# Kernel tuning notes

Hardware: AMD Instinct MI355X
Metric: run time of the kernel (lower is better)

## Reference

```python
import jax, jax.numpy as jnp
import numpy as np

STRIDE, PADDING, EPS = 2, 1, 1e-5


def setup_inputs() -> dict:
    key = jax.random.key(0)
    k1, k2, k3 = jax.random.split(key, 3)
    C_in, C_out, K = 64, 64, 4
    x = jax.random.normal(k1, (32, C_in, 64, 64), dtype=jnp.float32)
    weight = jax.random.normal(k2, (C_in, C_out, K, K), dtype=jnp.float32) * 0.05  # torch layout (in,out,kh,kw)
    conv_bias = jax.random.normal(k3, (C_out,), dtype=jnp.float32) * 0.02
    gamma = jnp.ones((C_out,), dtype=jnp.float32)
    beta = jnp.zeros((C_out,), dtype=jnp.float32)
    running_mean = jnp.zeros((C_out,), dtype=jnp.float32)
    running_var = jnp.ones((C_out,), dtype=jnp.float32)
    return {"x": x, "weight": weight, "conv_bias": conv_bias, "gamma": gamma,
            "beta": beta, "running_mean": running_mean, "running_var": running_var}


def _conv_transpose2d(x, weight, bias, stride, padding):
    # torch.nn.functional.conv_transpose2d equivalent:
    # conv with lhs_dilation=stride, spatially-flipped kernel, in/out axes swapped,
    # and padding k-1-p on each side.
    k = weight.shape[2]
    w_t = jnp.transpose(jnp.flip(weight, (2, 3)), (1, 0, 2, 3))  # (Cout, Cin, k, k)
    pad = k - 1 - padding
    y = jax.lax.conv_general_dilated(
        x, w_t,
        window_strides=(1, 1),
        padding=[(pad, pad), (pad, pad)],
        lhs_dilation=(stride, stride),
        dimension_numbers=("NCHW", "OIHW", "NCHW"),
    )
    return y + bias[None, :, None, None]


def reference(x, weight, conv_bias, gamma, beta, running_mean, running_var):
    # ConvTranspose2d
    y = _conv_transpose2d(x, weight, conv_bias, STRIDE, PADDING)  # [N,C,128,128]
    # BatchNorm2d (inference, running stats)
    scale = gamma * jax.lax.rsqrt(running_var + EPS)
    y = (y - running_mean[None, :, None, None]) * scale[None, :, None, None] + beta[None, :, None, None]
    # Softmax over channel dim
    y = jax.nn.softmax(y, axis=1)
    # MaxPool2d(k=2, s=2): H,W are even, so reshape-max is exact
    N, C, H, W = y.shape
    y = y.reshape(N, C, H // 2, 2, W // 2, 2).max(axis=(3, 5))  # [N,C,64,64]
    return y
```

## Files before the change

kernel.cpp:

```cpp
#include <hip/hip_runtime.h>
#include <hip/hip_bf16.h>
#include <math.h>


typedef __attribute__((ext_vector_type(8))) short short8;
typedef __attribute__((ext_vector_type(4))) float floatx4;
typedef __attribute__((ext_vector_type(2))) unsigned uint2v;

__device__ ushort g_wfrag[4 * 8 * 4 * 64 * 8];
__device__ float g_aff[64];

#define L2E 1.44269504088896340736f

__device__ __forceinline__ ushort f2bf(float f) {
  union { float f; unsigned u; } v; v.f = f;
  unsigned r = v.u + 0x7FFF + ((v.u >> 16) & 1);
  return (ushort)(r >> 16);
}

__global__ __launch_bounds__(256) void prep_kernel(
    const float* __restrict__ w, const float* __restrict__ bias,
    const float* __restrict__ gamma, const float* __restrict__ beta,
    const float* __restrict__ mean, const float* __restrict__ var) {
  int t = blockIdx.x * 256 + threadIdx.x;
  int cin0 = (t >> 6) * 2;
  int cout = t & 63;
  int nt = cout >> 4, b15 = cout & 15;
  int q = (cin0 & 31) >> 3;
  int j = cin0 & 7;
  int ksq = cin0 >> 5;
  float Aw = gamma[cout] * rsqrtf(var[cout] + 1e-5f) * L2E;

  const float4* p0 = (const float4*)&w[(cin0 * 64 + cout) * 16];
  const float4* p1 = (const float4*)&w[((cin0 + 1) * 64 + cout) * 16];
  float a[16], b[16];
  {
    float4 f0 = p0[0], f1 = p0[1], f2 = p0[2], f3 = p0[3];
    a[0]=f0.x; a[1]=f0.y; a[2]=f0.z; a[3]=f0.w; a[4]=f1.x; a[5]=f1.y; a[6]=f1.z; a[7]=f1.w;
    a[8]=f2.x; a[9]=f2.y; a[10]=f2.z; a[11]=f2.w; a[12]=f3.x; a[13]=f3.y; a[14]=f3.z; a[15]=f3.w;
    float4 g0 = p1[0], g1 = p1[1], g2 = p1[2], g3 = p1[3];
    b[0]=g0.x; b[1]=g0.y; b[2]=g0.z; b[3]=g0.w; b[4]=g1.x; b[5]=g1.y; b[6]=g1.z; b[7]=g1.w;
    b[8]=g2.x; b[9]=g2.y; b[10]=g2.z; b[11]=g2.w; b[12]=g3.x; b[13]=g3.y; b[14]=g3.z; b[15]=g3.w;
  }
#pragma unroll
  for (int kh = 0; kh < 4; ++kh)
#pragma unroll
    for (int kw = 0; kw < 4; ++kw) {
      int r = (kh & 1) ? 0 : 1;
      int pp = (kw & 1) ? 0 : 1;
      int c = r * 2 + pp;
      int tap = (kh >> 1) * 2 + (kw >> 1);
      int ks = tap * 2 + ksq;
      unsigned u = (unsigned)f2bf(a[kh * 4 + kw] * Aw) |
                   ((unsigned)f2bf(b[kh * 4 + kw] * Aw) << 16);
      *(unsigned*)&g_wfrag[(((c * 8 + ks) * 4 + nt) * 64 + q * 16 + b15) * 8 + j] = u;
    }

  if (t < 64) {
    float A0 = gamma[t] * rsqrtf(var[t] + 1e-5f);
    g_aff[t] = ((bias[t] - mean[t]) * A0 + beta[t]) * L2E;
  }
}

__device__ __forceinline__ unsigned cvtpk(float a, float b) {
  unsigned r;
  asm("v_cvt_pk_bf16_f32 %0, %1, %2" : "=v"(r) : "v"(a), "v"(b));
  return r;
}

template <int CTRL>
__device__ __forceinline__ float dpp_add(float v) {
  unsigned t = (unsigned)__builtin_amdgcn_update_dpp(
      0, (int)__float_as_uint(v), CTRL, 0xF, 0xF, true);
  return v + __uint_as_float(t);
}

__device__ __forceinline__ float sum16(float v) {
  v = dpp_add<0xB1>(v);
  v = dpp_add<0x4E>(v);
  v = dpp_add<0x141>(v);
  v = dpp_add<0x140>(v);
  return v;
}

__device__ __forceinline__ float fexp2(float x) {
#if __has_builtin(__builtin_amdgcn_exp2f)
  return __builtin_amdgcn_exp2f(x);
#else
  return exp2f(x);
#endif
}

__device__ __forceinline__ void gload_lds16(const void* g, void* l) {
  __builtin_amdgcn_global_load_lds(
      (const __attribute__((address_space(1))) void*)g,
      (__attribute__((address_space(3))) void*)l, 16, 0, 0);
}

#define COLS 66
#define ROWSTRIDE (COLS * 64)

__global__ __launch_bounds__(512, 4) void fused_kernel(const float* __restrict__ x,
                                                       float* __restrict__ out) {
  __shared__ __align__(16) ushort xs[4 * ROWSTRIDE];
  __shared__ __align__(16) float red[2 * 64 * 65 + 16];

  ushort* wbuf = (ushort*)red;

  const int tid  = threadIdx.x;
  const int swz  = ((blockIdx.x & 7) << 2) | (blockIdx.x >> 3);
  const int ph0  = swz * 2;
  const int n    = blockIdx.y;
  const int wave = tid >> 6;
  const int lane = tid & 63;
  const int b15  = lane & 15;
  const int q    = lane >> 4;
  const int wc   = wave & 1;
  const int c    = wave >> 1;
  const int r    = c >> 1, p = c & 1;

#define STAGE_W(ks_)                                                          \
  {                                                                           \
    _Pragma("unroll")                                                         \
    for (int nt_ = 0; nt_ < 4; ++nt_)                                         \
      gload_lds16(&g_wfrag[(((c * 8 + (ks_)) * 4 + nt_) * 64 + lane) * 8],    \
                  &wbuf[(wave * 4 + nt_) * 512]);                             \
  }
  STAGE_W(0);

  for (int e = tid; e < 1024; e += 512) {
    int iw4 = e & 15;
    int c4  = (e >> 4) & 15;
    int row = e >> 8;
    int ih  = ph0 - 1 + row;
    float4 v0 = {0.f, 0.f, 0.f, 0.f}, v1 = v0, v2 = v0, v3 = v0;
    if (ih >= 0 && ih < 64) {
      const float* xp = x + ((n * 64 + c4 * 4) * 64 + ih) * 64 + iw4 * 4;
      v0 = *(const float4*)xp;          v1 = *(const float4*)(xp + 4096);
      v2 = *(const float4*)(xp + 8192); v3 = *(const float4*)(xp + 12288);
    }
    int chunk = c4 >> 1, half4 = (c4 & 1) * 4;
    float cc[4][4] = {{v0.x, v1.x, v2.x, v3.x}, {v0.y, v1.y, v2.y, v3.y},
                      {v0.z, v1.z, v2.z, v3.z}, {v0.w, v1.w, v2.w, v3.w}};
#pragma unroll
    for (int ii = 0; ii < 4; ++ii) {
      int col = iw4 * 4 + ii + 1;
      uint2v pk = {cvtpk(cc[ii][0], cc[ii][1]), cvtpk(cc[ii][2], cc[ii][3])};
      *(uint2v*)&xs[(row * COLS + col) * 64 + ((chunk ^ (col & 7)) * 8) + half4] = pk;
    }
  }
  for (int e = tid; e < 128; e += 512) {
    int c4 = e & 15, side = (e >> 4) & 1, row = e >> 5;
    int col = side ? 65 : 0;
    int chunk = c4 >> 1, half4 = (c4 & 1) * 4;
    ushort4 z; z.x = z.y = z.z = z.w = 0;
    *(ushort4*)&xs[(row * COLS + col) * 64 + ((chunk ^ (col & 7)) * 8) + half4] = z;
  }

  float Dc[4];
#pragma unroll
  for (int nt = 0; nt < 4; ++nt) Dc[nt] = g_aff[nt * 16 + b15];

  int A2[2][2];
#pragma unroll
  for (int b = 0; b < 2; ++b) {
    int col = wc * 32 + b15 + (b ? p - 1 : p) + 1;
#pragma unroll
    for (int par = 0; par < 2; ++par)
      A2[b][par] = r * ROWSTRIDE + col * 64 + (((par * 4 + q) ^ (col & 7)) * 8);
  }

  __syncthreads();

  floatx4 acc[16];
#pragma unroll
  for (int i = 0; i < 16; ++i) {
    float d = Dc[i & 3];
    acc[i] = (floatx4){d, d, d, d};
  }

#pragma unroll
  for (int ks = 0; ks < 8; ++ks) {
    asm volatile("s_waitcnt vmcnt(0)" ::: "memory");
    short8 bf[4];
#pragma unroll
    for (int nt = 0; nt < 4; ++nt)
      bf[nt] = *(const short8*)&wbuf[(wave * 4 + nt) * 512 + lane * 8];
    const int b_ = (ks >> 1) & 1, par_ = ks & 1;
    const int ro = (ks >> 2) ? 0 : ROWSTRIDE;
    const int base = A2[b_][par_] + ro;
    short8 af00 = *(const short8*)&xs[base];
    short8 af01 = *(const short8*)&xs[base + 1024];
    short8 af10 = *(const short8*)&xs[base + ROWSTRIDE];
    short8 af11 = *(const short8*)&xs[base + ROWSTRIDE + 1024];
    asm volatile("s_waitcnt lgkmcnt(0)" ::: "memory");
    if (ks < 7) STAGE_W(ks + 1);
#pragma unroll
    for (int nt = 0; nt < 4; ++nt) {
      acc[nt]      = __builtin_amdgcn_mfma_f32_16x16x32_bf16(af00, bf[nt], acc[nt], 0, 0, 0);
      acc[4 + nt]  = __builtin_amdgcn_mfma_f32_16x16x32_bf16(af01, bf[nt], acc[4 + nt], 0, 0, 0);
      acc[8 + nt]  = __builtin_amdgcn_mfma_f32_16x16x32_bf16(af10, bf[nt], acc[8 + nt], 0, 0, 0);
      acc[12 + nt] = __builtin_amdgcn_mfma_f32_16x16x32_bf16(af11, bf[nt], acc[12 + nt], 0, 0, 0);
    }
  }

#pragma unroll
  for (int prow = 0; prow < 2; ++prow)
#pragma unroll
    for (int mt = 0; mt < 2; ++mt) {
      float sm[4] = {0.f, 0.f, 0.f, 0.f};
#pragma unroll
      for (int nt = 0; nt < 4; ++nt)
#pragma unroll
        for (int reg = 0; reg < 4; ++reg) {
          float e = fexp2(acc[prow * 8 + mt * 4 + nt][reg]);
          acc[prow * 8 + mt * 4 + nt][reg] = e;
          sm[reg] += e;
        }
#pragma unroll
      for (int reg = 0; reg < 4; ++reg)
        sm[reg] = __builtin_amdgcn_rcpf(sum16(sm[reg]));
#pragma unroll
      for (int nt = 0; nt < 4; ++nt)
#pragma unroll
        for (int reg = 0; reg < 4; ++reg)
          acc[prow * 8 + mt * 4 + nt][reg] *= sm[reg];
    }

  __syncthreads();

  if (c == 0) {
#pragma unroll
    for (int prow = 0; prow < 2; ++prow)
#pragma unroll
      for (int mt = 0; mt < 2; ++mt)
#pragma unroll
        for (int nt = 0; nt < 4; ++nt) {
          int idx = (prow * 64 + nt * 16 + b15) * 65 + wc * 32 + q * 8 + mt * 4;
#pragma unroll
          for (int reg = 0; reg < 4; ++reg)
            red[idx + reg] = acc[prow * 8 + mt * 4 + nt][reg];
        }
  }
  __syncthreads();
  if (c != 0) {
#pragma unroll
    for (int prow = 0; prow < 2; ++prow)
#pragma unroll
      for (int mt = 0; mt < 2; ++mt)
#pragma unroll
        for (int nt = 0; nt < 4; ++nt) {
          int idx = (prow * 64 + nt * 16 + b15) * 65 + wc * 32 + q * 8 + mt * 4;
#pragma unroll
          for (int reg = 0; reg < 4; ++reg)
            __hip_atomic_fetch_max((unsigned*)&red[idx + reg],
                                   __float_as_uint(acc[prow * 8 + mt * 4 + nt][reg]),
                                   __ATOMIC_RELAXED, __HIP_MEMORY_SCOPE_WORKGROUP);
        }
  }
  __syncthreads();

  for (int e = tid; e < 4096; e += 512) {
    int pw2  = e & 31;
    int cout = (e >> 5) & 63;
    int rl   = e >> 11;
    int pw   = pw2 * 2;
    int Lh   = pw & 31;
    int phys = ((pw >> 5) << 5) | (((Lh >> 2) & 3) << 3) | (((Lh >> 4) & 1) << 2) | (Lh & 3);
    int base = (rl * 64 + cout) * 65 + phys;
    float2 val = {red[base], red[base + 1]};
    *(float2*)&out[((n * 64 + cout) * 64 + (ph0 + rl)) * 64 + pw] = val;
  }
}

extern "C" void kernel_launch(void* const* d_in, const int* in_sizes, int n_in,
                              void* d_out, int out_size, void* d_ws, size_t ws_size,
                              hipStream_t stream) {
  const float* x     = (const float*)d_in[0];
  const float* w     = (const float*)d_in[1];
  const float* bias  = (const float*)d_in[2];
  const float* gamma = (const float*)d_in[3];
  const float* beta  = (const float*)d_in[4];
  const float* mean  = (const float*)d_in[5];
  const float* var   = (const float*)d_in[6];
  float* out = (float*)d_out;

  prep_kernel<<<8, 256, 0, stream>>>(w, bias, gamma, beta, mean, var);
  dim3 grid(32, 32);
  fused_kernel<<<grid, 512, 0, stream>>>(x, out);
}
```

Measured before the change: 113.4 us.

## Process two row tiles per block and prefetch the next input tile

Each block now covers four pooled output rows in two passes instead of two rows in one pass, and the grid is halved to match. While the first tile's softmax runs, the input rows for the second tile are loaded from global memory into registers. After the barrier they are packed into shared memory, hiding part of the global load latency. The costs are more registers, a serialized second pass per block, fewer blocks to spread across CUs, and a reload of the overlapping halo rows instead of reusing them.

```diff
diff --git a/kernel.cpp b/kernel.cpp
--- a/kernel.cpp
+++ b/kernel.cpp
@@ -108,8 +108,8 @@
   ushort* wbuf = (ushort*)red;
 
   const int tid  = threadIdx.x;
-  const int swz  = ((blockIdx.x & 7) << 2) | (blockIdx.x >> 3);
-  const int ph0  = swz * 2;
+  const int phg  = ((blockIdx.x & 7) << 1) | (blockIdx.x >> 3);
+  const int P    = phg * 4;
   const int n    = blockIdx.y;
   const int wave = tid >> 6;
   const int lane = tid & 63;
@@ -126,28 +126,35 @@
       gload_lds16(&g_wfrag[(((c * 8 + (ks_)) * 4 + nt_) * 64 + lane) * 8],    \
                   &wbuf[(wave * 4 + nt_) * 512]);                             \
   }
+
+#define PACK_WRITE(e_, v0_, v1_, v2_, v3_)                                    \
+  {                                                                           \
+    int iw4_ = (e_)&15, c4_ = ((e_) >> 4) & 15, row_ = (e_) >> 8;             \
+    int chunk_ = c4_ >> 1, half4_ = (c4_ & 1) * 4;                            \
+    float cc_[4][4] = {{v0_.x, v1_.x, v2_.x, v3_.x}, {v0_.y, v1_.y, v2_.y, v3_.y}, \
+                       {v0_.z, v1_.z, v2_.z, v3_.z}, {v0_.w, v1_.w, v2_.w, v3_.w}}; \
+    _Pragma("unroll")                                                         \
+    for (int ii_ = 0; ii_ < 4; ++ii_) {                                       \
+      int col_ = iw4_ * 4 + ii_ + 1;                                          \
+      uint2v pk_ = {cvtpk(cc_[ii_][0], cc_[ii_][1]), cvtpk(cc_[ii_][2], cc_[ii_][3])}; \
+      *(uint2v*)&xs[(row_ * COLS + col_) * 64 + ((chunk_ ^ (col_ & 7)) * 8) + half4_] = pk_; \
+    }                                                                         \
+  }
+
   STAGE_W(0);
 
-  for (int e = tid; e < 1024; e += 512) {
-    int iw4 = e & 15;
-    int c4  = (e >> 4) & 15;
-    int row = e >> 8;
-    int ih  = ph0 - 1 + row;
+#pragma unroll
+  for (int it = 0; it < 2; ++it) {
+    int e = tid + it * 512;
+    int iw4 = e & 15, c4 = (e >> 4) & 15, row = e >> 8;
+    int ih = P - 1 + row;
     float4 v0 = {0.f, 0.f, 0.f, 0.f}, v1 = v0, v2 = v0, v3 = v0;
     if (ih >= 0 && ih < 64) {
       const float* xp = x + ((n * 64 + c4 * 4) * 64 + ih) * 64 + iw4 * 4;
       v0 = *(const float4*)xp;          v1 = *(const float4*)(xp + 4096);
       v2 = *(const float4*)(xp + 8192); v3 = *(const float4*)(xp + 12288);
     }
-    int chunk = c4 >> 1, half4 = (c4 & 1) * 4;
-    float cc[4][4] = {{v0.x, v1.x, v2.x, v3.x}, {v0.y, v1.y, v2.y, v3.y},
-                      {v0.z, v1.z, v2.z, v3.z}, {v0.w, v1.w, v2.w, v3.w}};
-#pragma unroll
-    for (int ii = 0; ii < 4; ++ii) {
-      int col = iw4 * 4 + ii + 1;
-      uint2v pk = {cvtpk(cc[ii][0], cc[ii][1]), cvtpk(cc[ii][2], cc[ii][3])};
-      *(uint2v*)&xs[(row * COLS + col) * 64 + ((chunk ^ (col & 7)) * 8) + half4] = pk;
-    }
+    PACK_WRITE(e, v0, v1, v2, v3);
   }
   for (int e = tid; e < 128; e += 512) {
     int c4 = e & 15, side = (e >> 4) & 1, row = e >> 5;
@@ -172,104 +179,137 @@
 
   __syncthreads();
 
-  floatx4 acc[16];
-#pragma unroll
-  for (int i = 0; i < 16; ++i) {
-    float d = Dc[i & 3];
-    acc[i] = (floatx4){d, d, d, d};
-  }
-
-#pragma unroll
-  for (int ks = 0; ks < 8; ++ks) {
-    asm volatile("s_waitcnt vmcnt(0)" ::: "memory");
-    short8 bf[4];
-#pragma unroll
-    for (int nt = 0; nt < 4; ++nt)
-      bf[nt] = *(const short8*)&wbuf[(wave * 4 + nt) * 512 + lane * 8];
-    const int b_ = (ks >> 1) & 1, par_ = ks & 1;
-    const int ro = (ks >> 2) ? 0 : ROWSTRIDE;
-    const int base = A2[b_][par_] + ro;
-    short8 af00 = *(const short8*)&xs[base];
-    short8 af01 = *(const short8*)&xs[base + 1024];
-    short8 af10 = *(const short8*)&xs[base + ROWSTRIDE];
-    short8 af11 = *(const short8*)&xs[base + ROWSTRIDE + 1024];
-    asm volatile("s_waitcnt lgkmcnt(0)" ::: "memory");
-    if (ks < 7) STAGE_W(ks + 1);
-#pragma unroll
-    for (int nt = 0; nt < 4; ++nt) {
-      acc[nt]      = __builtin_amdgcn_mfma_f32_16x16x32_bf16(af00, bf[nt], acc[nt], 0, 0, 0);
-      acc[4 + nt]  = __builtin_amdgcn_mfma_f32_16x16x32_bf16(af01, bf[nt], acc[4 + nt], 0, 0, 0);
-      acc[8 + nt]  = __builtin_amdgcn_mfma_f32_16x16x32_bf16(af10, bf[nt], acc[8 + nt], 0, 0, 0);
-      acc[12 + nt] = __builtin_amdgcn_mfma_f32_16x16x32_bf16(af11, bf[nt], acc[12 + nt], 0, 0, 0);
-    }
-  }
-
-#pragma unroll
-  for (int prow = 0; prow < 2; ++prow)
-#pragma unroll
-    for (int mt = 0; mt < 2; ++mt) {
-      float sm[4] = {0.f, 0.f, 0.f, 0.f};
+#pragma unroll
+  for (int t = 0; t < 2; ++t) {
+    if (t == 1) STAGE_W(0);
+
+    floatx4 acc[16];
+#pragma unroll
+    for (int i = 0; i < 16; ++i) {
+      float d = Dc[i & 3];
+      acc[i] = (floatx4){d, d, d, d};
+    }
+
+#pragma unroll
+    for (int ks = 0; ks < 8; ++ks) {
+      asm volatile("s_waitcnt vmcnt(0)" ::: "memory");
+      short8 bf[4];
 #pragma unroll
       for (int nt = 0; nt < 4; ++nt)
-#pragma unroll
-        for (int reg = 0; reg < 4; ++reg) {
-          float e = fexp2(acc[prow * 8 + mt * 4 + nt][reg]);
-          acc[prow * 8 + mt * 4 + nt][reg] = e;
-          sm[reg] += e;
+        bf[nt] = *(const short8*)&wbuf[(wave * 4 + nt) * 512 + lane * 8];
+      const int b_ = (ks >> 1) & 1, par_ = ks & 1;
+      const int ro = (ks >> 2) ? 0 : ROWSTRIDE;
+      const int base = A2[b_][par_] + ro;
+      short8 af00 = *(const short8*)&xs[base];
+      short8 af01 = *(const short8*)&xs[base + 1024];
+      short8 af10 = *(const short8*)&xs[base + ROWSTRIDE];
+      short8 af11 = *(const short8*)&xs[base + ROWSTRIDE + 1024];
+      asm volatile("s_waitcnt lgkmcnt(0)" ::: "memory");
+      if (ks < 7) STAGE_W(ks + 1);
+#pragma unroll
+      for (int nt = 0; nt < 4; ++nt) {
+        acc[nt]      = __builtin_amdgcn_mfma_f32_16x16x32_bf16(af00, bf[nt], acc[nt], 0, 0, 0);
+        acc[4 + nt]  = __builtin_amdgcn_mfma_f32_16x16x32_bf16(af01, bf[nt], acc[4 + nt], 0, 0, 0);
+        acc[8 + nt]  = __builtin_amdgcn_mfma_f32_16x16x32_bf16(af10, bf[nt], acc[8 + nt], 0, 0, 0);
+        acc[12 + nt] = __builtin_amdgcn_mfma_f32_16x16x32_bf16(af11, bf[nt], acc[12 + nt], 0, 0, 0);
+      }
+    }
+
+#pragma unroll
+    for (int prow = 0; prow < 2; ++prow)
+#pragma unroll
+      for (int mt = 0; mt < 2; ++mt) {
+        float sm[4] = {0.f, 0.f, 0.f, 0.f};
+#pragma unroll
+        for (int nt = 0; nt < 4; ++nt)
+#pragma unroll
+          for (int reg = 0; reg < 4; ++reg) {
+            float e = fexp2(acc[prow * 8 + mt * 4 + nt][reg]);
+            acc[prow * 8 + mt * 4 + nt][reg] = e;
+            sm[reg] += e;
+          }
+#pragma unroll
+        for (int reg = 0; reg < 4; ++reg)
+          sm[reg] = __builtin_amdgcn_rcpf(sum16(sm[reg]));
+#pragma unroll
+        for (int nt = 0; nt < 4; ++nt)
+#pragma unroll
+          for (int reg = 0; reg < 4; ++reg)
+            acc[prow * 8 + mt * 4 + nt][reg] *= sm[reg];
+      }
+
+    float4 t2v[2][4];
+    if (t == 0) {
+#pragma unroll
+      for (int it = 0; it < 2; ++it) {
+        int e = tid + it * 512;
+        int iw4 = e & 15, c4 = (e >> 4) & 15, row = e >> 8;
+        int ih = P + 1 + row;
+        float4 z = {0.f, 0.f, 0.f, 0.f};
+        t2v[it][0] = z; t2v[it][1] = z; t2v[it][2] = z; t2v[it][3] = z;
+        if (ih < 64) {
+          const float* xp = x + ((n * 64 + c4 * 4) * 64 + ih) * 64 + iw4 * 4;
+          t2v[it][0] = *(const float4*)xp;          t2v[it][1] = *(const float4*)(xp + 4096);
+          t2v[it][2] = *(const float4*)(xp + 8192); t2v[it][3] = *(const float4*)(xp + 12288);
         }
-#pragma unroll
-      for (int reg = 0; reg < 4; ++reg)
-        sm[reg] = __builtin_amdgcn_rcpf(sum16(sm[reg]));
-#pragma unroll
-      for (int nt = 0; nt < 4; ++nt)
-#pragma unroll
-        for (int reg = 0; reg < 4; ++reg)
-          acc[prow * 8 + mt * 4 + nt][reg] *= sm[reg];
-    }
-
-  __syncthreads();
-
-  if (c == 0) {
-#pragma unroll
-    for (int prow = 0; prow < 2; ++prow)
-#pragma unroll
-      for (int mt = 0; mt < 2; ++mt)
-#pragma unroll
-        for (int nt = 0; nt < 4; ++nt) {
-          int idx = (prow * 64 + nt * 16 + b15) * 65 + wc * 32 + q * 8 + mt * 4;
-#pragma unroll
-          for (int reg = 0; reg < 4; ++reg)
-            red[idx + reg] = acc[prow * 8 + mt * 4 + nt][reg];
-        }
-  }
-  __syncthreads();
-  if (c != 0) {
-#pragma unroll
-    for (int prow = 0; prow < 2; ++prow)
-#pragma unroll
-      for (int mt = 0; mt < 2; ++mt)
-#pragma unroll
-        for (int nt = 0; nt < 4; ++nt) {
-          int idx = (prow * 64 + nt * 16 + b15) * 65 + wc * 32 + q * 8 + mt * 4;
-#pragma unroll
-          for (int reg = 0; reg < 4; ++reg)
-            __hip_atomic_fetch_max((unsigned*)&red[idx + reg],
-                                   __float_as_uint(acc[prow * 8 + mt * 4 + nt][reg]),
-                                   __ATOMIC_RELAXED, __HIP_MEMORY_SCOPE_WORKGROUP);
-        }
-  }
-  __syncthreads();
-
-  for (int e = tid; e < 4096; e += 512) {
-    int pw2  = e & 31;
-    int cout = (e >> 5) & 63;
-    int rl   = e >> 11;
-    int pw   = pw2 * 2;
-    int Lh   = pw & 31;
-    int phys = ((pw >> 5) << 5) | (((Lh >> 2) & 3) << 3) | (((Lh >> 4) & 1) << 2) | (Lh & 3);
-    int base = (rl * 64 + cout) * 65 + phys;
-    float2 val = {red[base], red[base + 1]};
-    *(float2*)&out[((n * 64 + cout) * 64 + (ph0 + rl)) * 64 + pw] = val;
+      }
+    }
+
+    __syncthreads();
+
+    if (t == 0) {
+#pragma unroll
+      for (int it = 0; it < 2; ++it) {
+        int e = tid + it * 512;
+        PACK_WRITE(e, t2v[it][0], t2v[it][1], t2v[it][2], t2v[it][3]);
+      }
+    }
+
+    if (c == 0) {
+#pragma unroll
+      for (int prow = 0; prow < 2; ++prow)
+#pragma unroll
+        for (int mt = 0; mt < 2; ++mt)
+#pragma unroll
+          for (int nt = 0; nt < 4; ++nt) {
+            int idx = (prow * 64 + nt * 16 + b15) * 65 + wc * 32 + q * 8 + mt * 4;
+#pragma unroll
+            for (int reg = 0; reg < 4; ++reg)
+              red[idx + reg] = acc[prow * 8 + mt * 4 + nt][reg];
+          }
+    }
+    __syncthreads();
+    if (c != 0) {
+#pragma unroll
+      for (int prow = 0; prow < 2; ++prow)
+#pragma unroll
+        for (int mt = 0; mt < 2; ++mt)
+#pragma unroll
+          for (int nt = 0; nt < 4; ++nt) {
+            int idx = (prow * 64 + nt * 16 + b15) * 65 + wc * 32 + q * 8 + mt * 4;
+#pragma unroll
+            for (int reg = 0; reg < 4; ++reg)
+              __hip_atomic_fetch_max((unsigned*)&red[idx + reg],
+                                     __float_as_uint(acc[prow * 8 + mt * 4 + nt][reg]),
+                                     __ATOMIC_RELAXED, __HIP_MEMORY_SCOPE_WORKGROUP);
+          }
+    }
+    __syncthreads();
+
+    const int ph0 = P + 2 * t;
+    for (int e = tid; e < 4096; e += 512) {
+      int pw2  = e & 31;
+      int cout = (e >> 5) & 63;
+      int rl   = e >> 11;
+      int pw   = pw2 * 2;
+      int Lh   = pw & 31;
+      int phys = ((pw >> 5) << 5) | (((Lh >> 2) & 3) << 3) | (((Lh >> 4) & 1) << 2) | (Lh & 3);
+      int base = (rl * 64 + cout) * 65 + phys;
+      float2 val = {red[base], red[base + 1]};
+      *(float2*)&out[((n * 64 + cout) * 64 + (ph0 + rl)) * 64 + pw] = val;
+    }
+
+    if (t == 0) __syncthreads();
   }
 }
 
@@ -286,6 +326,6 @@
   float* out = (float*)d_out;
 
   prep_kernel<<<8, 256, 0, stream>>>(w, bias, gamma, beta, mean, var);
-  dim3 grid(32, 32);
+  dim3 grid(16, 32);
   fused_kernel<<<grid, 512, 0, stream>>>(x, out);
 }
```

Measured after the change: 152.7 us. 1.35x slower.
